# Optimization experiments

Measured on AMD Instinct MI355X. Metric: run time of the kernel, lower is better.

Reference implementation:

```python
import jax, jax.numpy as jnp
import numpy as np

EMBED_DIM = 1024
PROJ_DIM = 256


def setup_inputs() -> dict:
    key = jax.random.key(0)
    kx, kq, kk = jax.random.split(key, 3)
    x = jax.random.normal(kx, (8, 4096, EMBED_DIM), dtype=jnp.float32)
    scale = 1.0 / (PROJ_DIM ** 0.5)
    q_proj = jax.random.normal(kq, (EMBED_DIM, PROJ_DIM), dtype=jnp.float32) * scale
    k_proj = jax.random.normal(kk, (EMBED_DIM, PROJ_DIM), dtype=jnp.float32) * scale
    return {"x": x, "q_proj": q_proj, "k_proj": k_proj}


def reference(x, q_proj, k_proj):
    # exp feature maps (FAVOR-style)
    q_prime = jnp.exp(jnp.einsum('bld,de->ble', x, q_proj))  # [B, L, E]
    k_prime = jnp.exp(jnp.einsum('bld,de->ble', x, k_proj))  # [B, L, E]
    # associative KV summary: O(L*E*D)
    kv = jnp.einsum('ble,bld->bed', k_prime, x)               # [B, E, D]
    num = jnp.einsum('ble,bed->bld', q_prime, kv)             # [B, L, D]
    z = 1.0 / (jnp.sum(q_prime, axis=-1, keepdims=True) + 1e-8)
    return num * z
```

## Files before the change

kernel.cpp:

```cpp
#include <hip/hip_runtime.h>


#define EMBED 1024
#define PROJ  256
#define LSEQ  4096
#define BATCH 8

typedef short  bfrag __attribute__((ext_vector_type(8)));
typedef float  f4    __attribute__((ext_vector_type(4)));
typedef unsigned short u16x8 __attribute__((ext_vector_type(8)));
typedef unsigned short u16x4 __attribute__((ext_vector_type(4)));

static __device__ __forceinline__ unsigned short f2bf(float f) {
  unsigned int u = __builtin_bit_cast(unsigned int, f);
  u += 0x7fffu + ((u >> 16) & 1u);
  return (unsigned short)(u >> 16);
}
static __device__ __forceinline__ float bf2f(unsigned short h) {
  unsigned int u = ((unsigned int)h) << 16;
  return __builtin_bit_cast(float, u);
}

static __device__ __forceinline__ void gload_lds16(const void* g, void* l) {
  __builtin_amdgcn_global_load_lds(
      (__attribute__((address_space(1))) void*)(unsigned long long)(g),
      (__attribute__((address_space(3))) void*)(unsigned)(unsigned long long)(l),
      16, 0, 0);
}

static __device__ __forceinline__ void stage_tile(
    const unsigned short* __restrict__ src, int row0, int stride, int k0,
    unsigned short* lds, int wave, int lane) {
#pragma unroll
  for (int j = 0; j < 4; j++) {
    int slot = (wave * 4 + j) * 64 + lane;
    int r = slot >> 3, cp = slot & 7;
    int c = cp ^ (r & 7);
    gload_lds16(src + (size_t)(row0 + r) * stride + k0 + c * 8,
                lds + (wave * 4 + j) * 512);
  }
}

static __device__ __forceinline__ bfrag read_frag(const unsigned short* lds,
                                                  int row, int chunk) {
  return *(const bfrag*)(lds + ((row << 3) + (chunk ^ (row & 7))) * 8);
}

__global__ __launch_bounds__(256) void cvtx_kernel(
    const float* __restrict__ x, unsigned short* __restrict__ xb,
    unsigned short* __restrict__ xT) {
  __shared__ unsigned short T[64 * 64];
  const int tid = threadIdx.x;
  const int d0 = blockIdx.x * 64, l0 = blockIdx.y * 64, b = blockIdx.z;
#pragma unroll
  for (int it = 0; it < 4; it++) {
    int slot = it * 256 + tid;
    int r = slot >> 4, c4 = slot & 15;
    const size_t row = (size_t)(b * LSEQ + l0 + r) * EMBED + d0 + c4 * 4;
    f4 v = *(const f4*)(x + row);
    u16x4 hv = (u16x4){f2bf(v[0]), f2bf(v[1]), f2bf(v[2]), f2bf(v[3])};
    *(u16x4*)(xb + row) = hv;
    const int g = ((r >> 2) ^ c4) << 2;
#pragma unroll
    for (int j = 0; j < 4; j++)
      T[(c4 * 4 + j) * 64 + g + (r & 3)] = hv[j];
  }
  __syncthreads();
#pragma unroll
  for (int it = 0; it < 2; it++) {
    int slot = it * 256 + tid;
    int dd = slot >> 3, ch = slot & 7;
    int q = dd >> 2;
    u16x4 lo = *(const u16x4*)(T + dd * 64 + (((2 * ch) ^ q) << 2));
    u16x4 hi = *(const u16x4*)(T + dd * 64 + (((2 * ch + 1) ^ q) << 2));
    u16x8 o = (u16x8){lo[0], lo[1], lo[2], lo[3], hi[0], hi[1], hi[2], hi[3]};
    *(u16x8*)(xT + ((size_t)(b * EMBED + d0 + dd)) * LSEQ + l0 + ch * 8) = o;
  }
}

__global__ __launch_bounds__(256) void cvtw_kernel(
    const float* __restrict__ qw, const float* __restrict__ kw,
    unsigned short* __restrict__ wt) {
  __shared__ unsigned short T[64][72];
  const int tid = threadIdx.x;
  const int n0 = blockIdx.x * 64, k0 = blockIdx.y * 64;
  const float* W = blockIdx.z ? kw : qw;
#pragma unroll
  for (int it = 0; it < 4; it++) {
    int slot = it * 256 + tid;
    int r = slot >> 4, c4 = slot & 15;
    f4 v = *(const f4*)(W + (size_t)(k0 + r) * PROJ + n0 + c4 * 4);
#pragma unroll
    for (int j = 0; j < 4; j++) T[c4 * 4 + j][r] = f2bf(v[j]);
  }
  __syncthreads();
#pragma unroll
  for (int it = 0; it < 2; it++) {
    int slot = it * 256 + tid;
    int n = slot >> 3, ch = slot & 7;
    *(u16x8*)(wt + ((size_t)(blockIdx.z * PROJ + n0 + n)) * EMBED + k0 + ch * 8) =
        *(const u16x8*)&T[n][ch * 8];
  }
}

__global__ __launch_bounds__(256) void proj_kernel(
    const unsigned short* __restrict__ xb, const unsigned short* __restrict__ wt,
    unsigned short* __restrict__ qp, unsigned short* __restrict__ kT) {
  __shared__ union {
    struct { unsigned short A[128 * 64]; unsigned short B[128 * 64]; } t;
    unsigned short T[128 * 136];
  } sm;
  const int tid = threadIdx.x, wave = tid >> 6, lane = tid & 63;
  const int quad = lane >> 4, l16 = lane & 15;
  const int wm = wave >> 1, wn = wave & 1;
  const int n0 = blockIdx.x * 128, m0 = blockIdx.y * 128;

  f4 acc[4][4];
#pragma unroll
  for (int i = 0; i < 4; i++)
#pragma unroll
    for (int j = 0; j < 4; j++) acc[i][j] = (f4){0.f, 0.f, 0.f, 0.f};

  for (int k0 = 0; k0 < EMBED; k0 += 64) {
    stage_tile(xb, m0, EMBED, k0, sm.t.A, wave, lane);
    stage_tile(wt, n0, EMBED, k0, sm.t.B, wave, lane);
    __syncthreads();
#pragma unroll
    for (int ks = 0; ks < 2; ks++) {
      bfrag a[4], bfr[4];
#pragma unroll
      for (int mt = 0; mt < 4; mt++)
        a[mt] = read_frag(sm.t.A, wm * 64 + mt * 16 + l16, ks * 4 + quad);
#pragma unroll
      for (int nt = 0; nt < 4; nt++)
        bfr[nt] = read_frag(sm.t.B, wn * 64 + nt * 16 + l16, ks * 4 + quad);
#pragma unroll
      for (int mt = 0; mt < 4; mt++)
#pragma unroll
        for (int nt = 0; nt < 4; nt++)
          acc[mt][nt] = __builtin_amdgcn_mfma_f32_16x16x32_bf16(
              a[mt], bfr[nt], acc[mt][nt], 0, 0, 0);
    }
    __syncthreads();
  }

  if (n0 < PROJ) {
#pragma unroll
    for (int mt = 0; mt < 4; mt++)
#pragma unroll
      for (int nt = 0; nt < 4; nt++)
#pragma unroll
        for (int r = 0; r < 4; r++)
          sm.T[(wm * 64 + mt * 16 + quad * 4 + r) * 136 + wn * 64 + nt * 16 + l16] =
              f2bf(__expf(acc[mt][nt][r]));
    __syncthreads();
#pragma unroll
    for (int it = 0; it < 8; it++) {
      int slot = it * 256 + tid;
      int row = slot >> 4, ch = slot & 15;
      *(u16x8*)(qp + (size_t)(m0 + row) * PROJ + n0 + ch * 8) =
          *(const u16x8*)&sm.T[row * 136 + ch * 8];
    }
  } else {
#pragma unroll
    for (int mt = 0; mt < 4; mt++)
#pragma unroll
      for (int nt = 0; nt < 4; nt++) {
        u16x4 h;
#pragma unroll
        for (int r = 0; r < 4; r++) h[r] = f2bf(__expf(acc[mt][nt][r]));
        *(u16x4*)&sm.T[(wn * 64 + nt * 16 + l16) * 136 + wm * 64 + mt * 16 + quad * 4] = h;
      }
    __syncthreads();
    const int bb = m0 >> 12, l0 = m0 & 4095, ebase = n0 - PROJ;
#pragma unroll
    for (int it = 0; it < 8; it++) {
      int slot = it * 256 + tid;
      int e = slot >> 4, ch = slot & 15;
      *(u16x8*)(kT + (size_t)(bb * PROJ + ebase + e) * LSEQ + l0 + ch * 8) =
          *(const u16x8*)&sm.T[e * 136 + ch * 8];
    }
  }
}

__global__ __launch_bounds__(256) void zinv_kernel(
    const unsigned short* __restrict__ qp, float* __restrict__ zinv) {
  int m = blockIdx.x * 4 + (threadIdx.x >> 6);
  int lane = threadIdx.x & 63;
  u16x4 h = *(const u16x4*)(qp + (size_t)m * PROJ + lane * 4);
  float s = bf2f(h[0]) + bf2f(h[1]) + bf2f(h[2]) + bf2f(h[3]);
#pragma unroll
  for (int off = 32; off; off >>= 1) s += __shfl_xor(s, off);
  if (lane == 0) zinv[m] = 1.0f / (s + 1e-8f);
}

__global__ __launch_bounds__(256) void kv_kernel(
    const unsigned short* __restrict__ kT, const unsigned short* __restrict__ xT,
    float* __restrict__ kvp) {
  __shared__ struct { unsigned short A[128 * 64]; unsigned short B[128 * 64]; } sm;
  const int tid = threadIdx.x, wave = tid >> 6, lane = tid & 63;
  const int quad = lane >> 4, l16 = lane & 15;
  const int wm = wave >> 1, wn = wave & 1;
  const int d0 = blockIdx.x * 128, e0 = blockIdx.y * 128;
  const int b = blockIdx.z & 7, split = blockIdx.z >> 3;
  const unsigned short* As = kT + (size_t)b * PROJ * LSEQ;
  const unsigned short* Bs = xT + (size_t)b * EMBED * LSEQ;

  f4 acc[4][4];
#pragma unroll
  for (int i = 0; i < 4; i++)
#pragma unroll
    for (int j = 0; j < 4; j++) acc[i][j] = (f4){0.f, 0.f, 0.f, 0.f};

  const int kbase = split * 1024;
  for (int kk = 0; kk < 1024; kk += 64) {
    stage_tile(As, e0, LSEQ, kbase + kk, sm.A, wave, lane);
    stage_tile(Bs, d0, LSEQ, kbase + kk, sm.B, wave, lane);
    __syncthreads();
#pragma unroll
    for (int ks = 0; ks < 2; ks++) {
      bfrag a[4], bfr[4];
#pragma unroll
      for (int mt = 0; mt < 4; mt++)
        a[mt] = read_frag(sm.A, wm * 64 + mt * 16 + l16, ks * 4 + quad);
#pragma unroll
      for (int nt = 0; nt < 4; nt++)
        bfr[nt] = read_frag(sm.B, wn * 64 + nt * 16 + l16, ks * 4 + quad);
#pragma unroll
      for (int mt = 0; mt < 4; mt++)
#pragma unroll
        for (int nt = 0; nt < 4; nt++)
          acc[mt][nt] = __builtin_amdgcn_mfma_f32_16x16x32_bf16(
              a[mt], bfr[nt], acc[mt][nt], 0, 0, 0);
    }
    __syncthreads();
  }

#pragma unroll
  for (int mt = 0; mt < 4; mt++)
#pragma unroll
    for (int nt = 0; nt < 4; nt++)
#pragma unroll
      for (int r = 0; r < 4; r++) {
        int e = e0 + wm * 64 + mt * 16 + quad * 4 + r;
        int d = d0 + wn * 64 + nt * 16 + l16;
        kvp[((size_t)(split * 8 + b) * PROJ + e) * EMBED + d] = acc[mt][nt][r];
      }
}

__global__ __launch_bounds__(256) void kvreduce_kernel(
    const float* __restrict__ kvp, unsigned short* __restrict__ kvT) {
  __shared__ float T[64][68];
  const int tid = threadIdx.x;
  const int d0 = blockIdx.x * 64, e0 = blockIdx.y * 64, b = blockIdx.z;
#pragma unroll
  for (int it = 0; it < 4; it++) {
    int slot = it * 256 + tid;
    int e = slot >> 4, c4 = slot & 15;
    f4 s = (f4){0.f, 0.f, 0.f, 0.f};
#pragma unroll
    for (int sp = 0; sp < 4; sp++)
      s += *(const f4*)(kvp + ((size_t)(sp * 8 + b) * PROJ + e0 + e) * EMBED + d0 + c4 * 4);
#pragma unroll
    for (int j = 0; j < 4; j++) T[c4 * 4 + j][e] = s[j];
  }
  __syncthreads();
#pragma unroll
  for (int it = 0; it < 2; it++) {
    int slot = it * 256 + tid;
    int d = slot >> 3, ch = slot & 7;
    u16x8 h;
#pragma unroll
    for (int j = 0; j < 8; j++) h[j] = f2bf(T[d][ch * 8 + j]);
    *(u16x8*)(kvT + ((size_t)(b * EMBED + d0 + d)) * PROJ + e0 + ch * 8) = h;
  }
}

__global__ __launch_bounds__(256) void out_kernel(
    const unsigned short* __restrict__ qp, const unsigned short* __restrict__ kvT,
    const float* __restrict__ zinv, float* __restrict__ out) {
  __shared__ struct { unsigned short A[128 * 64]; unsigned short B[128 * 64]; } sm;
  __shared__ float zv[128];
  const int tid = threadIdx.x, wave = tid >> 6, lane = tid & 63;
  const int quad = lane >> 4, l16 = lane & 15;
  const int wm = wave >> 1, wn = wave & 1;
  const int d0 = blockIdx.x * 128, l0 = blockIdx.y * 128, b = blockIdx.z;
  const unsigned short* As = qp + (size_t)b * LSEQ * PROJ;
  const unsigned short* Bs = kvT + (size_t)b * EMBED * PROJ;

  if (tid < 128) zv[tid] = zinv[b * LSEQ + l0 + tid];

  f4 acc[4][4];
#pragma unroll
  for (int i = 0; i < 4; i++)
#pragma unroll
    for (int j = 0; j < 4; j++) acc[i][j] = (f4){0.f, 0.f, 0.f, 0.f};

  for (int k0 = 0; k0 < PROJ; k0 += 64) {
    stage_tile(As, l0, PROJ, k0, sm.A, wave, lane);
    stage_tile(Bs, d0, PROJ, k0, sm.B, wave, lane);
    __syncthreads();
#pragma unroll
    for (int ks = 0; ks < 2; ks++) {
      bfrag a[4], bfr[4];
#pragma unroll
      for (int mt = 0; mt < 4; mt++)
        a[mt] = read_frag(sm.A, wm * 64 + mt * 16 + l16, ks * 4 + quad);
#pragma unroll
      for (int nt = 0; nt < 4; nt++)
        bfr[nt] = read_frag(sm.B, wn * 64 + nt * 16 + l16, ks * 4 + quad);
#pragma unroll
      for (int mt = 0; mt < 4; mt++)
#pragma unroll
        for (int nt = 0; nt < 4; nt++)
          acc[mt][nt] = __builtin_amdgcn_mfma_f32_16x16x32_bf16(
              a[mt], bfr[nt], acc[mt][nt], 0, 0, 0);
    }
    __syncthreads();
  }

#pragma unroll
  for (int mt = 0; mt < 4; mt++)
#pragma unroll
    for (int nt = 0; nt < 4; nt++)
#pragma unroll
      for (int r = 0; r < 4; r++) {
        int row = wm * 64 + mt * 16 + quad * 4 + r;
        int d = d0 + wn * 64 + nt * 16 + l16;
        out[((size_t)(b * LSEQ + l0 + row)) * EMBED + d] = acc[mt][nt][r] * zv[row];
      }
}

extern "C" void kernel_launch(void* const* d_in, const int* in_sizes, int n_in,
                              void* d_out, int out_size, void* d_ws, size_t ws_size,
                              hipStream_t stream) {
  const float* x  = (const float*)d_in[0];
  const float* qw = (const float*)d_in[1];
  const float* kw = (const float*)d_in[2];
  float* out = (float*)d_out;

  char* ws = (char*)d_ws;
  unsigned short* xb   = (unsigned short*)(ws);
  unsigned short* xT   = (unsigned short*)(ws + 67108864);
  unsigned short* wt   = (unsigned short*)(ws + 134217728);
  unsigned short* qp   = (unsigned short*)(ws + 135266304);
  unsigned short* kT   = (unsigned short*)(ws + 152043520);
  unsigned short* kvT  = (unsigned short*)(ws + 168820736);
  float*          zinv = (float*)(ws + 173015040);
  float*          kvp  = (float*)(ws);

  cvtx_kernel<<<dim3(16, 64, 8), 256, 0, stream>>>(x, xb, xT);
  cvtw_kernel<<<dim3(4, 16, 2), 256, 0, stream>>>(qw, kw, wt);
  proj_kernel<<<dim3(4, 256), 256, 0, stream>>>(xb, wt, qp, kT);
  zinv_kernel<<<dim3(8192), 256, 0, stream>>>(qp, zinv);
  kv_kernel<<<dim3(8, 2, 32), 256, 0, stream>>>(kT, xT, kvp);
  kvreduce_kernel<<<dim3(16, 4, 8), 256, 0, stream>>>(kvp, kvT);
  out_kernel<<<dim3(8, 32, 8), 256, 0, stream>>>(qp, kvT, zinv, out);
}
```

Measured before the change: 388.8 us.

## Store bf16 intermediates in 64x64 blocked tiles for contiguous tile staging

The bf16 copies of x, its transpose, and the transposed k-feature matrix are now written as contiguous 64x64 blobs instead of row-major arrays. The GEMM kernels stage LDS tiles from these blobs, so each 64-wide tile row is read from one contiguous 8KB region rather than strided rows. This aims to improve DRAM/TLB locality and coalescing for global_load_lds. It changes the layout contract between the producer and consumer kernels, so any unconverted reader in the hidden code would break.

```diff
diff --git a/kernel.cpp b/kernel.cpp
--- a/kernel.cpp
+++ b/kernel.cpp
@@ -41,6 +41,20 @@
   }
 }
 
+static __device__ __forceinline__ void stage_tile_blk(
+    const unsigned short* __restrict__ src, int row0, int ntcols, int k0,
+    unsigned short* lds, int wave, int lane) {
+#pragma unroll
+  for (int j = 0; j < 4; j++) {
+    int slot = (wave * 4 + j) * 64 + lane;
+    int r = slot >> 3, cp = slot & 7;
+    int c = cp ^ (r & 7);
+    const unsigned short* blob =
+        src + ((((size_t)(row0 >> 6) + (r >> 6)) * ntcols + (k0 >> 6)) << 12);
+    gload_lds16(blob + ((r & 63) << 6) + c * 8, lds + (wave * 4 + j) * 512);
+  }
+}
+
 static __device__ __forceinline__ bfrag read_frag(const unsigned short* lds,
                                                   int row, int chunk) {
   return *(const bfrag*)(lds + ((row << 3) + (chunk ^ (row & 7))) * 8);
@@ -52,14 +66,16 @@
   __shared__ unsigned short T[64 * 64];
   const int tid = threadIdx.x;
   const int d0 = blockIdx.x * 64, l0 = blockIdx.y * 64, b = blockIdx.z;
+  const int mt = (b * LSEQ + l0) >> 6, dt = d0 >> 6;
+  unsigned short* xbB = xb + (((size_t)mt * 16 + dt) << 12);
+  unsigned short* xTB = xT + ((((size_t)b * 16 + dt) * 64 + (l0 >> 6)) << 12);
 #pragma unroll
   for (int it = 0; it < 4; it++) {
     int slot = it * 256 + tid;
     int r = slot >> 4, c4 = slot & 15;
-    const size_t row = (size_t)(b * LSEQ + l0 + r) * EMBED + d0 + c4 * 4;
-    f4 v = *(const f4*)(x + row);
+    f4 v = *(const f4*)(x + (size_t)(b * LSEQ + l0 + r) * EMBED + d0 + c4 * 4);
     u16x4 hv = (u16x4){f2bf(v[0]), f2bf(v[1]), f2bf(v[2]), f2bf(v[3])};
-    *(u16x4*)(xb + row) = hv;
+    *(u16x4*)(xbB + r * 64 + c4 * 4) = hv;
     const int g = ((r >> 2) ^ c4) << 2;
 #pragma unroll
     for (int j = 0; j < 4; j++)
@@ -74,7 +90,7 @@
     u16x4 lo = *(const u16x4*)(T + dd * 64 + (((2 * ch) ^ q) << 2));
     u16x4 hi = *(const u16x4*)(T + dd * 64 + (((2 * ch + 1) ^ q) << 2));
     u16x8 o = (u16x8){lo[0], lo[1], lo[2], lo[3], hi[0], hi[1], hi[2], hi[3]};
-    *(u16x8*)(xT + ((size_t)(b * EMBED + d0 + dd)) * LSEQ + l0 + ch * 8) = o;
+    *(u16x8*)(xTB + dd * 64 + ch * 8) = o;
   }
 }
 
@@ -122,7 +138,7 @@
     for (int j = 0; j < 4; j++) acc[i][j] = (f4){0.f, 0.f, 0.f, 0.f};
 
   for (int k0 = 0; k0 < EMBED; k0 += 64) {
-    stage_tile(xb, m0, EMBED, k0, sm.t.A, wave, lane);
+    stage_tile_blk(xb, m0, 16, k0, sm.t.A, wave, lane);
     stage_tile(wt, n0, EMBED, k0, sm.t.B, wave, lane);
     __syncthreads();
 #pragma unroll
@@ -172,13 +188,17 @@
         *(u16x4*)&sm.T[(wn * 64 + nt * 16 + l16) * 136 + wm * 64 + mt * 16 + quad * 4] = h;
       }
     __syncthreads();
-    const int bb = m0 >> 12, l0 = m0 & 4095, ebase = n0 - PROJ;
+    const int bb = m0 >> 12, l0w = m0 & 4095, ebase = n0 - PROJ;
 #pragma unroll
     for (int it = 0; it < 8; it++) {
-      int slot = it * 256 + tid;
-      int e = slot >> 4, ch = slot & 15;
-      *(u16x8*)(kT + (size_t)(bb * PROJ + ebase + e) * LSEQ + l0 + ch * 8) =
-          *(const u16x8*)&sm.T[e * 136 + ch * 8];
+      int cid = it * 256 + tid;
+      int blobi = cid >> 9, within = cid & 511;
+      int er = within >> 3, ch = within & 7;
+      int e = (blobi >> 1) * 64 + er, lc = (blobi & 1) * 8 + ch;
+      unsigned short* blob =
+          kT + ((((size_t)bb * 4 + ((ebase >> 6) + (blobi >> 1))) * 64 +
+                 (l0w >> 6) + (blobi & 1)) << 12);
+      *(u16x8*)(blob + (er << 6) + ch * 8) = *(const u16x8*)&sm.T[e * 136 + lc * 8];
     }
   }
 }
@@ -203,8 +223,8 @@
   const int wm = wave >> 1, wn = wave & 1;
   const int d0 = blockIdx.x * 128, e0 = blockIdx.y * 128;
   const int b = blockIdx.z & 7, split = blockIdx.z >> 3;
-  const unsigned short* As = kT + (size_t)b * PROJ * LSEQ;
-  const unsigned short* Bs = xT + (size_t)b * EMBED * LSEQ;
+  const unsigned short* As = kT + ((size_t)b * 4 * 64 << 12);
+  const unsigned short* Bs = xT + ((size_t)b * 16 * 64 << 12);
 
   f4 acc[4][4];
 #pragma unroll
@@ -214,8 +234,8 @@
 
   const int kbase = split * 1024;
   for (int kk = 0; kk < 1024; kk += 64) {
-    stage_tile(As, e0, LSEQ, kbase + kk, sm.A, wave, lane);
-    stage_tile(Bs, d0, LSEQ, kbase + kk, sm.B, wave, lane);
+    stage_tile_blk(As, e0, 64, kbase + kk, sm.A, wave, lane);
+    stage_tile_blk(Bs, d0, 64, kbase + kk, sm.B, wave, lane);
     __syncthreads();
 #pragma unroll
     for (int ks = 0; ks < 2; ks++) {
```

New measurement: 386.4 us. Within noise of the previous version (-0.6%).
